# Optimization experiments

Hardware: AMD Instinct MI355X
Metric: run time of the kernel (lower is better)

Reference implementation:

```python
import jax, jax.numpy as jnp
from jax import lax
import numpy as np

D_MODEL = 1024
D_STATE = 64
D_CONV = 4
EXPAND = 2
HEADDIM = 64
D_INNER = EXPAND * D_MODEL          # 2048
NHEADS = D_INNER // HEADDIM         # 32
CHUNK = 64
CONV_DIM = D_INNER + 2 * D_STATE    # 2176
D_IN_PROJ = 2 * D_INNER + 2 * D_STATE + NHEADS  # 4256
B_SZ = 4
SEQLEN = 2048
EPS = 1e-5


def _silu(x):
    return x * jax.nn.sigmoid(x)


def _segsum(x):
    # x: [..., T]; returns [..., T, T] with [i,j] = sum_{j<k<=i} x[k], -inf above diag
    T = x.shape[-1]
    xe = jnp.broadcast_to(x[..., None], x.shape + (T,))
    strict_lower = jnp.tril(jnp.ones((T, T), bool), -1)
    xe = jnp.where(strict_lower, xe, 0.0)
    s = jnp.cumsum(xe, axis=-2)
    lower = jnp.tril(jnp.ones((T, T), bool), 0)
    return jnp.where(lower, s, -jnp.inf)


def setup_inputs() -> dict:
    key = jax.random.key(0)
    ks = jax.random.split(key, 5)
    u = jax.random.normal(ks[0], (B_SZ, SEQLEN, D_MODEL), jnp.float32)
    W_in = jax.random.normal(ks[1], (D_IN_PROJ, D_MODEL), jnp.float32) * 0.02
    conv_w = jax.random.normal(ks[2], (CONV_DIM, 1, D_CONV), jnp.float32) * 0.2  # depthwise kernel
    conv_b = jnp.zeros((CONV_DIM,), jnp.float32)
    dt_bias = jax.random.uniform(ks[3], (NHEADS,), jnp.float32, -1.0, 1.0)
    A_log = jnp.log(jnp.linspace(1.0, float(NHEADS), NHEADS)).astype(jnp.float32)
    D = jnp.ones((NHEADS,), jnp.float32)
    norm_w = jnp.ones((D_INNER,), jnp.float32)
    W_out = jax.random.normal(ks[4], (D_MODEL, D_INNER), jnp.float32) * 0.02
    return dict(u=u, W_in=W_in, conv_w=conv_w, conv_b=conv_b, dt_bias=dt_bias,
                A_log=A_log, D=D, norm_w=norm_w, W_out=W_out)


def reference(u, W_in, conv_w, conv_b, dt_bias, A_log, D, norm_w, W_out):
    b, s, _ = u.shape
    A = -jnp.exp(A_log)                                   # [H]
    zxbcdt = u @ W_in.T                                   # [b,s,D_IN_PROJ]
    z = zxbcdt[..., :D_INNER]
    xBC = zxbcdt[..., D_INNER:D_INNER + CONV_DIM]
    dt = jax.nn.softplus(zxbcdt[..., D_INNER + CONV_DIM:] + dt_bias)  # [b,s,H]

    # causal depthwise conv1d (left pad d_conv-1 == torch pad-both + slice[:s])
    xc = lax.conv_general_dilated(
        xBC.transpose(0, 2, 1), conv_w, window_strides=(1,),
        padding=[(D_CONV - 1, 0)], feature_group_count=CONV_DIM,
        dimension_numbers=('NCH', 'OIH', 'NCH'))
    xBC = _silu(xc.transpose(0, 2, 1) + conv_b)           # [b,s,CONV_DIM]

    x = xBC[..., :D_INNER].reshape(b, s, NHEADS, HEADDIM)
    Bm = xBC[..., D_INNER:D_INNER + D_STATE]              # [b,s,N]
    Cm = xBC[..., D_INNER + D_STATE:]                     # [b,s,N]

    # SSD chunked scan
    nch = s // CHUNK
    xs = (x * dt[..., None]).reshape(b, nch, CHUNK, NHEADS, HEADDIM)
    Ad = (A * dt).reshape(b, nch, CHUNK, NHEADS)
    Br = Bm.reshape(b, nch, CHUNK, D_STATE)
    Cr = Cm.reshape(b, nch, CHUNK, D_STATE)
    A_ch = Ad.transpose(0, 1, 3, 2)                       # [b,c,h,l]
    A_cum = jnp.cumsum(A_ch, axis=-1)
    L = jnp.exp(_segsum(A_ch))                            # [b,c,h,l,l]
    Y_diag = jnp.einsum('bcln,bcsn,bchls,bcshp->bclhp', Cr, Br, L, xs)
    decay_states = jnp.exp(A_cum[..., -1:] - A_cum)       # [b,c,h,l]
    states = jnp.einsum('bchl,bcln,bclhp->bchpn', decay_states, Br, xs)
    init = jnp.zeros((b, 1, NHEADS, HEADDIM, D_STATE), xs.dtype)
    states = jnp.concatenate([init, states], axis=1)      # [b,c+1,h,p,n]
    total_decay = jnp.pad(A_cum[..., -1].transpose(0, 2, 1), ((0, 0), (0, 0), (1, 0)))
    decay_chunk = jnp.exp(_segsum(total_decay))           # [b,h,c+1,c+1]
    new_states = jnp.einsum('bhzc,bchpn->bzhpn', decay_chunk, states)
    states = new_states[:, :-1]                           # [b,c,h,p,n]
    state_decay_out = jnp.exp(A_cum)
    Y_off = jnp.einsum('bcln,bchpn,bchl->bclhp', Cr, states, state_decay_out)
    y = (Y_diag + Y_off).reshape(b, s, NHEADS, HEADDIM)

    y = y + x * D[:, None]
    y = y.reshape(b, s, D_INNER)
    # gated RMSNorm
    y = y * _silu(z)
    y = y * lax.rsqrt(jnp.mean(y * y, axis=-1, keepdims=True) + EPS) * norm_w
    return y @ W_out.T
```

## Files before the change

### kernel.cpp

```cpp
#include <hip/hip_runtime.h>
#include <hip/hip_bf16.h>

#define BSZ 4
#define SEQ 2048
#define DMODEL 1024
#define DINNER 2048
#define DSTATE 64
#define NH 32
#define HD 64
#define CKL 64
#define NCH 32
#define CONVD 2176
#define DPROJ 4256
#define N1 4224
#define MTOT 8192
#define YSTR 72
#define YSTR2 120
#define CVTB 6272

typedef __hip_bfloat16 bf16;
typedef __attribute__((ext_vector_type(8))) short short8;
typedef __attribute__((ext_vector_type(4))) short short4_;
typedef __attribute__((ext_vector_type(4))) float f32x4;

__device__ __forceinline__ float sigmoidf_(float x) { return 1.0f / (1.0f + __expf(-x)); }
__device__ __forceinline__ float bits2f(short s) { return __uint_as_float(((unsigned)(unsigned short)s) << 16); }
__device__ __forceinline__ short f2bits(float f) {
    bf16 h = __float2bfloat16(f);
    return *reinterpret_cast<short*>(&h);
}

__device__ __forceinline__ void gl_lds16(const bf16* g, bf16* l) {
    __builtin_amdgcn_global_load_lds((const __attribute__((address_space(1))) void*)g,
                                     (__attribute__((address_space(3))) void*)l, 16, 0, 0);
}

__device__ __forceinline__ f32x4 MF(short8 a, short8 b, f32x4 c) {
    return __builtin_amdgcn_mfma_f32_16x16x32_bf16(a, b, c, 0, 0, 0);
}

template<int N> __device__ __forceinline__ void vmw() {
    if constexpr (N == 0)      asm volatile("s_waitcnt vmcnt(0)" ::: "memory");
    else if constexpr (N == 3) asm volatile("s_waitcnt vmcnt(3)" ::: "memory");
    else if constexpr (N == 6) asm volatile("s_waitcnt vmcnt(6)" ::: "memory");
    else                       asm volatile("s_waitcnt vmcnt(15)" ::: "memory");
}

__device__ __forceinline__ void swzx(int& bx, int& by) {
    int nx = gridDim.x;
    int nwg = nx * gridDim.y;
    int Lr = blockIdx.y * nx + blockIdx.x;
    int L = (Lr & 7) * (nwg >> 3) + (Lr >> 3);
    int GSZ = nx * 8;
    int g = L / GSZ, r = L - g * GSZ;
    bx = r % nx;
    by = g * 8 + r / nx;
}

__global__ __launch_bounds__(256) void k_pre2(const float* __restrict__ u, const float* __restrict__ W_in,
                                              const float* __restrict__ dt_bias,
                                              const float* __restrict__ W_out, const float* __restrict__ nw,
                                              bf16* __restrict__ u_b, float* __restrict__ dtt,
                                              bf16* __restrict__ win_b, bf16* __restrict__ wout_b) {
    __shared__ __align__(16) float us[8 * DMODEL];
    const int tid = threadIdx.x;
    if (blockIdx.x < CVTB) {
        int g = (blockIdx.x * 256 + tid) * 4;
        if (g < N1 * DMODEL) {
            f32x4 f = *(const f32x4*)&W_in[g];
            short4_ o;
#pragma unroll
            for (int j = 0; j < 4; j++) o[j] = f2bits(f[j]);
            *(short4_*)&win_b[g] = o;
        } else if (g < N1 * DMODEL + DMODEL * DINNER) {
            int g2 = g - N1 * DMODEL;
            f32x4 f = *(const f32x4*)&W_out[g2];
            f32x4 w = *(const f32x4*)&nw[g2 & (DINNER - 1)];
            short4_ o;
#pragma unroll
            for (int j = 0; j < 4; j++) o[j] = f2bits(f[j] * w[j]);
            *(short4_*)&wout_b[g2] = o;
        }
        return;
    }
    const int t0 = (blockIdx.x - CVTB) * 8;
    const float* ur = u + (size_t)t0 * DMODEL;
    bf16* ub = u_b + (size_t)t0 * DMODEL;
#pragma unroll
    for (int i = 0; i < 8; i++) {
        int idx = (i * 256 + tid) * 4;
        f32x4 v = *(const f32x4*)&ur[idx];
        *(f32x4*)&us[idx] = v;
        short4_ o;
#pragma unroll
        for (int j = 0; j < 4; j++) o[j] = f2bits(v[j]);
        *(short4_*)&ub[idx] = o;
    }
    __syncthreads();
    const int h = tid >> 3, sub = tid & 7;
    const float* wr = W_in + (size_t)(DPROJ - NH + h) * DMODEL;
    float s[8] = {};
    for (int k = sub * 4; k < DMODEL; k += 32) {
        f32x4 w4 = *(const f32x4*)&wr[k];
#pragma unroll
        for (int rr = 0; rr < 8; rr++) {
            f32x4 u4 = *(const f32x4*)&us[rr * DMODEL + k];
            s[rr] += u4[0] * w4[0] + u4[1] * w4[1] + u4[2] * w4[2] + u4[3] * w4[3];
        }
    }
#pragma unroll
    for (int rr = 0; rr < 8; rr++) {
        s[rr] += __shfl_down(s[rr], 4, 8);
        s[rr] += __shfl_down(s[rr], 2, 8);
        s[rr] += __shfl_down(s[rr], 1, 8);
    }
    if (sub == 0) {
        float bh = dt_bias[h];
#pragma unroll
        for (int rr = 0; rr < 8; rr++) {
            float x = s[rr] + bh;
            dtt[(size_t)h * MTOT + t0 + rr] = (x > 20.f) ? x : log1pf(__expf(x));
        }
    }
}

__global__ __launch_bounds__(256) void k_dts(const float* __restrict__ dtt, const float* __restrict__ A_log,
                                             float* __restrict__ sAc, float* __restrict__ sfv,
                                             float* __restrict__ etot) {
    const int h = blockIdx.x, b = blockIdx.y;
    const int tid = threadIdx.x, w = tid >> 6, lane = tid & 63;
    const float Ah = -__expf(A_log[h]);
#pragma unroll
    for (int g = 0; g < 8; g++) {
        int c = g * 4 + w;
        int t0 = b * SEQ + c * CKL;
        float dv = dtt[(size_t)h * MTOT + t0 + lane];
        float v = Ah * dv;
#pragma unroll
        for (int d = 1; d < 64; d <<= 1) { float o = __shfl_up(v, d); if (lane >= d) v += o; }
        float tot = __shfl(v, 63);
        sAc[(size_t)h * MTOT + t0 + lane] = v;
        sfv[(size_t)h * MTOT + t0 + lane] = __expf(tot - v) * dv;
        if (lane == 63) etot[(h * BSZ + b) * NCH + c] = __expf(tot);
    }
}

#define BARWAIT()                                           \
    __builtin_amdgcn_s_barrier();                           \
    asm volatile("s_waitcnt lgkmcnt(0)" ::: "memory");      \
    __builtin_amdgcn_sched_barrier(0);                      \
    __builtin_amdgcn_s_setprio(1)
#define ENDPH()                                             \
    __builtin_amdgcn_s_setprio(0);                          \
    __builtin_amdgcn_s_barrier()

__global__ __launch_bounds__(512, 2) void k_g1(const bf16* __restrict__ Ap,
                                               const bf16* __restrict__ Wp,
                                               bf16* __restrict__ Cp) {
    __shared__ __align__(16) short sA[2][16384];
    __shared__ __align__(16) short sB[2][12288];
    const int tid = threadIdx.x;
    const int lane = tid & 63, w = tid >> 6;
    const int wm = w >> 2, wn = w & 3;
    const int lr = lane & 15, lk = lane >> 4;
    int bx, by; swzx(bx, by);
    const int m0 = by * 256, n0 = bx * 192;
    const int ld = DMODEL;

    const int r8 = tid >> 3;
    const int c8 = ((tid & 7) ^ (r8 & 7)) * 8;
    const bf16* pA = Ap + (size_t)(m0 + r8) * ld + c8;
    const bf16* pB = Wp + (size_t)(n0 + r8) * ld + c8;

    auto stA = [&](int d, int t) {
#pragma unroll
        for (int h = 0; h < 2; h++)
#pragma unroll
            for (int q = 0; q < 2; q++)
                gl_lds16(pA + (size_t)(h * 128 + q * 64) * ld + t * 64,
                         (bf16*)&sA[d][h * 8192 + q * 4096 + tid * 8]);
    };
    auto stB = [&](int d, int u, int t) {
        gl_lds16(pB + (size_t)(u * 64) * ld + t * 64,
                 (bf16*)&sB[d][u * 4096 + tid * 8]);
    };

    const int c0 = (lk ^ (lr & 7)) * 8;
    const int c1 = ((lk + 4) ^ (lr & 7)) * 8;
    const int aR = (wm * 128 + lr) * 64;
    const int bR = (wn * 48 + lr) * 64;

    f32x4 acc[8][3];
#pragma unroll
    for (int i = 0; i < 8; i++)
#pragma unroll
        for (int j = 0; j < 3; j++) acc[i][j] = (f32x4){0.f, 0.f, 0.f, 0.f};
    short8 bfr[3][2], af[2][2];

#define RDA1(D, I)                                                   \
    af[0][0] = *(const short8*)&sA[D][aR + (I) * 1024 + c0];         \
    af[0][1] = *(const short8*)&sA[D][aR + (I) * 1024 + c1];         \
    af[1][0] = *(const short8*)&sA[D][aR + (I + 1) * 1024 + c0];     \
    af[1][1] = *(const short8*)&sA[D][aR + (I + 1) * 1024 + c1]
#define RDB1(D)                                                      \
    _Pragma("unroll")                                                \
    for (int jn = 0; jn < 3; ++jn) {                                 \
        bfr[jn][0] = *(const short8*)&sB[D][bR + jn * 1024 + c0];    \
        bfr[jn][1] = *(const short8*)&sB[D][bR + jn * 1024 + c1];    \
    }
#define MM1(I)                                                       \
    _Pragma("unroll")                                                \
    for (int hh = 0; hh < 2; ++hh) {                                 \
        _Pragma("unroll")                                            \
        for (int jn = 0; jn < 3; ++jn) {                             \
            acc[I][jn]     = MF(af[0][hh], bfr[jn][hh], acc[I][jn]); \
            acc[I + 1][jn] = MF(af[1][hh], bfr[jn][hh], acc[I + 1][jn]); \
        }                                                            \
    }

    stB(0, 0, 0); stB(0, 1, 0); stB(0, 2, 0); stA(0, 0);
    stB(1, 0, 1); stB(1, 1, 1); stB(1, 2, 1);
    vmw<3>();
    __builtin_amdgcn_s_barrier();

    for (int t0 = 0; t0 < 16; t0 += 2) {
        const int t1 = t0 + 1, t2 = t0 + 2, t3 = t0 + 3;
        const bool more = (t2 < 16);
        RDB1(0); RDA1(0, 0);
        stA(1, t1);
        BARWAIT(); MM1(0); ENDPH();
        RDA1(0, 2); if (more) stB(0, 0, t2);
        BARWAIT(); MM1(2); ENDPH();
        RDA1(0, 4); if (more) stB(0, 1, t2);
        BARWAIT(); MM1(4); ENDPH();
        RDA1(0, 6); if (more) stB(0, 2, t2);
        BARWAIT(); MM1(6);
        __builtin_amdgcn_s_setprio(0);
        if (more) vmw<3>(); else vmw<0>();
        __builtin_amdgcn_s_barrier();
        RDB1(1); RDA1(1, 0);
        if (more) stA(0, t2);
        BARWAIT(); MM1(0); ENDPH();
        RDA1(1, 2); if (more) stB(1, 0, t3);
        BARWAIT(); MM1(2); ENDPH();
        RDA1(1, 4); if (more) stB(1, 1, t3);
        BARWAIT(); MM1(4); ENDPH();
        RDA1(1, 6); if (more) stB(1, 2, t3);
        BARWAIT(); MM1(6);
        __builtin_amdgcn_s_setprio(0);
        if (more) vmw<3>();
        __builtin_amdgcn_s_barrier();
    }
#undef RDA1
#undef RDB1
#undef MM1

#pragma unroll
    for (int im = 0; im < 8; im++) {
        int row = m0 + wm * 128 + im * 16 + lk * 4;
#pragma unroll
        for (int jn = 0; jn < 3; jn++) {
            int col = n0 + wn * 48 + jn * 16 + lr;
            bf16* cp = Cp + (size_t)row * N1 + col;
#pragma unroll
            for (int rr = 0; rr < 4; rr++) cp[(size_t)rr * N1] = __float2bfloat16(acc[im][jn][rr]);
        }
    }
}

__global__ __launch_bounds__(512, 2) void k_g2(const bf16* __restrict__ Ap,
                                               const bf16* __restrict__ Wp,
                                               float* __restrict__ Cp) {
    __shared__ __align__(16) short sA[3][16384];
    __shared__ __align__(16) short sB[3][8192];
    __shared__ float rsrow[256];
    const int tid = threadIdx.x;
    const int lane = tid & 63, w = tid >> 6;
    const int wm = w >> 1, wn = w & 1;
    const int lr = lane & 15, lk = lane >> 4;
    int bx, by; swzx(bx, by);
    const int m0 = by * 256, n0 = bx * 128;
    const int lda = N1, ldb = DINNER;

    const int r8 = tid >> 3;
    const int c8 = ((tid & 7) ^ (r8 & 7)) * 8;
    const bf16* pA = Ap + (size_t)(m0 + r8) * lda + c8;
    const bf16* pB = Wp + (size_t)(n0 + r8) * ldb + c8;

    auto stA = [&](int d, int t) {
#pragma unroll
        for (int h = 0; h < 2; h++)
#pragma unroll
            for (int q = 0; q < 2; q++)
                gl_lds16(pA + (size_t)(h * 128 + q * 64) * lda + t * 64,
                         (bf16*)&sA[d][h * 8192 + q * 4096 + tid * 8]);
    };
    auto stB = [&](int d, int t) {
#pragma unroll
        for (int q = 0; q < 2; q++)
            gl_lds16(pB + (size_t)(q * 64) * ldb + t * 64,
                     (bf16*)&sB[d][q * 4096 + tid * 8]);
    };

    const int c0 = (lk ^ (lr & 7)) * 8;
    const int c1 = ((lk + 4) ^ (lr & 7)) * 8;
    const int aR = (wm * 64 + lr) * 64;
    const int bR = (wn * 64 + lr) * 64;

    f32x4 acc[4][4];
#pragma unroll
    for (int i = 0; i < 4; i++)
#pragma unroll
        for (int j = 0; j < 4; j++) acc[i][j] = (f32x4){0.f, 0.f, 0.f, 0.f};
    float ssq[4] = {0.f, 0.f, 0.f, 0.f};
    short8 bfr[4][2], af[2][2];

#define RDA2(D, I)                                                   \
    af[0][0] = *(const short8*)&sA[D][aR + (I) * 1024 + c0];         \
    af[0][1] = *(const short8*)&sA[D][aR + (I) * 1024 + c1];         \
    af[1][0] = *(const short8*)&sA[D][aR + (I + 1) * 1024 + c0];     \
    af[1][1] = *(const short8*)&sA[D][aR + (I + 1) * 1024 + c1]
#define RDB2(D)                                                      \
    _Pragma("unroll")                                                \
    for (int jn = 0; jn < 4; ++jn) {                                 \
        bfr[jn][0] = *(const short8*)&sB[D][bR + jn * 1024 + c0];    \
        bfr[jn][1] = *(const short8*)&sB[D][bR + jn * 1024 + c1];    \
    }
#define MM2(I)                                                       \
    _Pragma("unroll")                                                \
    for (int hh = 0; hh < 2; ++hh) {                                 \
        _Pragma("unroll")                                            \
        for (int jn = 0; jn < 4; ++jn) {                             \
            acc[I][jn]     = MF(af[0][hh], bfr[jn][hh], acc[I][jn]); \
            acc[I + 1][jn] = MF(af[1][hh], bfr[jn][hh], acc[I + 1][jn]); \
        }                                                            \
    }
#define SSQ2(I)                                                      \
    _Pragma("unroll")                                                \
    for (int hh = 0; hh < 2; ++hh)                                   \
        _Pragma("unroll")                                            \
        for (int e = 0; e < 8; ++e) {                                \
            float v0 = bits2f(af[0][hh][e]), v1 = bits2f(af[1][hh][e]); \
            ssq[I] += v0 * v0; ssq[I + 1] += v1 * v1;                \
        }

    stB(0, 0); stA(0, 0);
    stB(1, 1); stA(1, 1);
    vmw<6>();
    __builtin_amdgcn_s_barrier();

    int rb = 0, sb = 2;
    for (int t = 0; t < 32; ++t) {
        const bool more = (t + 2 < 32);
        RDB2(rb); RDA2(rb, 0);
        if (more) stB(sb, t + 2);
        BARWAIT(); MM2(0); SSQ2(0); ENDPH();
        RDA2(rb, 2);
        if (more) stA(sb, t + 2);
        BARWAIT(); MM2(2); SSQ2(2);
        __builtin_amdgcn_s_setprio(0);
        if (more) vmw<6>(); else if (t + 1 < 32) vmw<0>();
        __builtin_amdgcn_s_barrier();
        rb = (rb == 2) ? 0 : rb + 1;
        sb = (sb == 2) ? 0 : sb + 1;
    }
#undef RDA2
#undef RDB2
#undef MM2
#undef SSQ2

#pragma unroll
    for (int im = 0; im < 4; im++) {
        float s = ssq[im];
        s += __shfl_down(s, 32);
        s += __shfl_down(s, 16);
        if (lane < 16) rsrow[wm * 64 + im * 16 + lane] = rsqrtf(s * (1.0f / DINNER) + 1e-5f);
    }
    __syncthreads();
#pragma unroll
    for (int im = 0; im < 4; im++) {
        int rl = wm * 64 + im * 16 + lk * 4;
        int row = m0 + rl;
#pragma unroll
        for (int rr = 0; rr < 4; rr++) {
            float s = rsrow[rl + rr];
#pragma unroll
            for (int jn = 0; jn < 4; jn++) {
                int col = n0 + wn * 64 + jn * 16 + lr;
                Cp[(size_t)(row + rr) * DMODEL + col] = acc[im][jn][rr] * s;
            }
        }
    }
}

__global__ __launch_bounds__(256) void k_conv(const bf16* __restrict__ zx, const float* __restrict__ cw,
                                              const float* __restrict__ cb, bf16* __restrict__ xbc) {
    const int g = blockIdx.x * 256 + threadIdx.x;
    const int c0 = (g % 544) * 4;
    const int t0 = (g / 544) * 4;
    const int s0 = t0 & (SEQ - 1);
    const short* base = (const short*)(zx + (size_t)t0 * N1 + DINNER + c0);
    f32x4 w0 = *(const f32x4*)&cw[(c0 + 0) * 4];
    f32x4 w1 = *(const f32x4*)&cw[(c0 + 1) * 4];
    f32x4 w2 = *(const f32x4*)&cw[(c0 + 2) * 4];
    f32x4 w3 = *(const f32x4*)&cw[(c0 + 3) * 4];
    f32x4 bias = *(const f32x4*)&cb[c0];
    short4_ v[7];
#pragma unroll
    for (int o = 0; o < 7; o++) {
        if (s0 + o - 3 >= 0) v[o] = *(const short4_*)(base + (long)(o - 3) * N1);
        else v[o] = (short4_){0, 0, 0, 0};
    }
#pragma unroll
    for (int j = 0; j < 4; j++) {
        f32x4 a = bias;
#pragma unroll
        for (int k = 0; k < 4; k++) {
            short4_ x = v[j + k];
            a[0] += bits2f(x[0]) * w0[k];
            a[1] += bits2f(x[1]) * w1[k];
            a[2] += bits2f(x[2]) * w2[k];
            a[3] += bits2f(x[3]) * w3[k];
        }
        short4_ o_;
#pragma unroll
        for (int jj = 0; jj < 4; jj++) o_[jj] = f2bits(a[jj] * sigmoidf_(a[jj]));
        *(short4_*)((short*)xbc + (size_t)(t0 + j) * CONVD + c0) = o_;
    }
}

__global__ __launch_bounds__(256) void k_ssd(const bf16* __restrict__ xbc, const float* __restrict__ dtt,
                                             const float* __restrict__ sAc, const float* __restrict__ sfv,
                                             const float* __restrict__ etg, const float* __restrict__ Dp,
                                             bf16* __restrict__ zx) {
    __shared__ __align__(16) short Ct[2][64 * YSTR];
    __shared__ __align__(16) short Bt[2][64 * YSTR];
    __shared__ __align__(16) short Bn[2][64 * YSTR2];
    __shared__ __align__(16) short Xt[2][32 * YSTR2];
    __shared__ __align__(16) short Sb[2][32 * YSTR];
    __shared__ __align__(16) short Gs[4 * 16 * YSTR];
    __shared__ __align__(16) float Sf[32 * 68];
    __shared__ __align__(16) float sdt2[2][64], sAc2[2][64];
    __shared__ float etl[NCH];

    const int ph = blockIdx.x, h = blockIdx.y, b = blockIdx.z;
    const int tid = threadIdx.x;
    const int lane = tid & 63, w = tid >> 6;
    const int lr = lane & 15, lk = lane >> 4;
    const float Dh = Dp[h];
    const int xcol = h * HD + ph * 32;

    const int lrow = tid >> 2, c0 = (tid & 3) * 16, px = (tid & 3) * 8;
    const int zl = 16 * w + (lane >> 2), zp = (lane & 3) * 8;

    short8 rC0, rC1, rB0, rB1, rX, rZ;
    float rdt, rsa, rsf;
    auto load_chunk = [&](int cc) {
        int rows0 = b * SEQ + cc * CKL;
        const short* rp = (const short*)(xbc + (size_t)(rows0 + lrow) * CONVD);
        rC0 = *(const short8*)&rp[DINNER + DSTATE + c0];
        rC1 = *(const short8*)&rp[DINNER + DSTATE + c0 + 8];
        rB0 = *(const short8*)&rp[DINNER + c0];
        rB1 = *(const short8*)&rp[DINNER + c0 + 8];
        rX  = *(const short8*)&rp[xcol + px];
        rZ  = *(const short8*)((const short*)zx + (size_t)(rows0 + zl) * N1 + xcol + zp);
        rdt = dtt[(size_t)h * MTOT + rows0 + lane];
        rsa = sAc[(size_t)h * MTOT + rows0 + lane];
        rsf = sfv[(size_t)h * MTOT + rows0 + lrow];
    };
    auto scatter = [&](int buf) {
        *(short8*)&Ct[buf][lrow * YSTR + c0] = rC0;
        *(short8*)&Ct[buf][lrow * YSTR + c0 + 8] = rC1;
        *(short8*)&Bt[buf][lrow * YSTR + c0] = rB0;
        *(short8*)&Bt[buf][lrow * YSTR + c0 + 8] = rB1;
#pragma unroll
        for (int j = 0; j < 8; j++) {
            int n0_ = c0 + j, n1_ = c0 + 8 + j, p_ = px + j;
            Bn[buf][n0_ * YSTR2 + lrow + (n0_ >> 3) * 8] = f2bits(bits2f(rB0[j]) * rsf);
            Bn[buf][n1_ * YSTR2 + lrow + (n1_ >> 3) * 8] = f2bits(bits2f(rB1[j]) * rsf);
            Xt[buf][p_ * YSTR2 + lrow + (p_ >> 3) * 8] = rX[j];
        }
        if (tid < 64) { sdt2[buf][tid] = rdt; sAc2[buf][tid] = rsa; }
    };

    for (int i = tid; i < 32 * 68; i += 256) Sf[i] = 0.f;
    for (int i = tid; i < 32 * YSTR; i += 256) Sb[0][i] = 0;
    if (tid < NCH) etl[tid] = etg[(h * BSZ + b) * NCH + tid];
    load_chunk(0);
    scatter(0);
    __syncthreads();

    for (int c = 0; c < NCH; c++) {
        const int par = c & 1, nb = par ^ 1;
        const int rows0 = b * SEQ + c * CKL;
        float etot = etl[c];
        short8 zcur = rZ;
        if (c + 1 < NCH) load_chunk(c + 1);

        short8 cf0 = *(const short8*)&Ct[par][(16 * w + lr) * YSTR + lk * 8];
        short8 cf1 = *(const short8*)&Ct[par][(16 * w + lr) * YSTR + 32 + lk * 8];
        f32x4 acc[2];
#pragma unroll
        for (int t = 0; t < 2; t++) {
            short8 s0 = *(const short8*)&Sb[par][(16 * t + lr) * YSTR + lk * 8];
            short8 s1 = *(const short8*)&Sb[par][(16 * t + lr) * YSTR + 32 + lk * 8];
            acc[t] = MF(cf0, s0, (f32x4){0.f, 0.f, 0.f, 0.f});
            acc[t] = MF(cf1, s1, acc[t]);
        }
        float sAcl[4], el[4];
#pragma unroll
        for (int rr = 0; rr < 4; rr++) { sAcl[rr] = sAc2[par][16 * w + lk * 4 + rr]; el[rr] = __expf(sAcl[rr]); }
#pragma unroll
        for (int t = 0; t < 2; t++)
#pragma unroll
            for (int rr = 0; rr < 4; rr++) acc[t][rr] *= el[rr];
        short* gw = Gs + w * 16 * YSTR;
#pragma unroll
        for (int t = 0; t < 4; t++) {
            short8 b0 = *(const short8*)&Bt[par][(16 * t + lr) * YSTR + lk * 8];
            short8 b1 = *(const short8*)&Bt[par][(16 * t + lr) * YSTR + 32 + lk * 8];
            f32x4 g = MF(cf0, b0, (f32x4){0.f, 0.f, 0.f, 0.f});
            g = MF(cf1, b1, g);
            int s = 16 * t + lr;
            float sAcs = sAc2[par][s], dts = sdt2[par][s];
#pragma unroll
            for (int rr = 0; rr < 4; rr++) {
                int l = 16 * w + lk * 4 + rr;
                float v = (s <= l) ? g[rr] * __expf(sAcl[rr] - sAcs) * dts : 0.f;
                gw[(lk * 4 + rr) * YSTR + s] = f2bits(v);
            }
        }
        short8 gf0 = *(const short8*)&gw[lr * YSTR + lk * 8];
        short8 gf1 = *(const short8*)&gw[lr * YSTR + 32 + lk * 8];
#pragma unroll
        for (int t = 0; t < 2; t++) {
            int xr = 16 * t + lr;
            short8 x0 = *(const short8*)&Xt[par][xr * YSTR2 + ((xr >> 3) + lk) * 8];
            short8 x1 = *(const short8*)&Xt[par][xr * YSTR2 + 32 + ((xr >> 3) + lk) * 8];
            acc[t] = MF(gf0, x0, acc[t]);
            acc[t] = MF(gf1, x1, acc[t]);
        }
        {
            int pw = w & 1, nh2 = w >> 1;
            const int xp = 16 * pw + lr;
            short8 xt0 = *(const short8*)&Xt[par][xp * YSTR2 + ((xp >> 3) + lk) * 8];
            short8 xt1 = *(const short8*)&Xt[par][xp * YSTR2 + 32 + ((xp >> 3) + lk) * 8];
#pragma unroll
            for (int j = 0; j < 2; j++) {
                int nt = 2 * nh2 + j;
                int nr = 16 * nt + lr;
                short8 b0 = *(const short8*)&Bn[par][nr * YSTR2 + ((nr >> 3) + lk) * 8];
                short8 b1 = *(const short8*)&Bn[par][nr * YSTR2 + 32 + ((nr >> 3) + lk) * 8];
                f32x4 sacc = MF(xt0, b0, (f32x4){0.f, 0.f, 0.f, 0.f});
                sacc = MF(xt1, b1, sacc);
#pragma unroll
                for (int rr = 0; rr < 4; rr++) {
                    int n = 16 * nt + lr;
                    int p = 16 * pw + lk * 4 + rr;
                    float nv = Sf[p * 68 + n] * etot + sacc[rr];
                    Sf[p * 68 + n] = nv;
                    Sb[nb][p * YSTR + n] = f2bits(nv);
                }
            }
        }
#pragma unroll
        for (int t = 0; t < 2; t++) {
#pragma unroll
            for (int rr = 0; rr < 4; rr++) {
                int p = 16 * t + lr;
                int l = 16 * w + lk * 4 + rr;
                float y = acc[t][rr] + Dh * bits2f(Xt[par][p * YSTR2 + l + (p >> 3) * 8]);
                Ct[par][l * YSTR + p] = f2bits(y);
            }
        }
        {
            short8 y8 = *(const short8*)&Ct[par][zl * YSTR + zp];
            short* zpp = (short*)zx + (size_t)(rows0 + zl) * N1 + xcol + zp;
            short8 o;
#pragma unroll
            for (int j = 0; j < 8; j++) {
                float z = bits2f(zcur[j]);
                o[j] = f2bits(bits2f(y8[j]) * (z * sigmoidf_(z)));
            }
            *(short8*)zpp = o;
        }
        if (c + 1 < NCH) {
            scatter(nb);
        }
        __syncthreads();
    }
}

extern "C" void kernel_launch(void* const* d_in, const int* in_sizes, int n_in,
                              void* d_out, int out_size, void* d_ws, size_t ws_size,
                              hipStream_t stream) {
    const float* u       = (const float*)d_in[0];
    const float* W_in    = (const float*)d_in[1];
    const float* conv_w  = (const float*)d_in[2];
    const float* conv_b  = (const float*)d_in[3];
    const float* dt_bias = (const float*)d_in[4];
    const float* A_log   = (const float*)d_in[5];
    const float* Dp      = (const float*)d_in[6];
    const float* norm_w  = (const float*)d_in[7];
    const float* W_out   = (const float*)d_in[8];
    float* out = (float*)d_out;

    char* ws = (char*)d_ws;
    bf16* zx     = (bf16*)ws;  ws += (size_t)MTOT * N1 * 2;
    bf16* xbc    = (bf16*)ws;  ws += (size_t)MTOT * CONVD * 2;
    bf16* wout_b = (bf16*)ws;  ws += (size_t)DMODEL * DINNER * 2;
    float* dtt   = (float*)ws; ws += (size_t)NH * MTOT * 4;
    float* sAcw  = (float*)ws; ws += (size_t)NH * MTOT * 4;
    float* sfvw  = (float*)ws; ws += (size_t)NH * MTOT * 4;
    float* etotw = (float*)ws; ws += 64 * 1024;

    bf16* u_b   = (bf16*)d_out;
    bf16* win_b = (bf16*)((char*)d_out + (size_t)MTOT * DMODEL * 2);

    k_pre2<<<CVTB + MTOT / 8, 256, 0, stream>>>(u, W_in, dt_bias, W_out, norm_w,
                                                u_b, dtt, win_b, wout_b);
    k_dts<<<dim3(NH, BSZ), 256, 0, stream>>>(dtt, A_log, sAcw, sfvw, etotw);

    k_g1<<<dim3(N1 / 192, MTOT / 256), 512, 0, stream>>>(u_b, win_b, zx);

    k_conv<<<(MTOT / 4) * (CONVD / 4) / 256, 256, 0, stream>>>(zx, conv_w, conv_b, xbc);

    k_ssd<<<dim3(2, NH, BSZ), 256, 0, stream>>>(xbc, dtt, sAcw, sfvw, etotw, Dp, zx);

    k_g2<<<dim3(DMODEL / 128, MTOT / 256), 512, 0, stream>>>(zx, wout_b, out);
}
```

Before: 376.7 us.

## Fuse x-channel depthwise conv into SSD kernel, keep separate conv only for B/C

The depthwise conv+SiLU for the x channels now runs inside the SSD kernel's chunk loader, reading four shifted rows of the projection output directly. The standalone conv kernel only processes the 128 B/C channels into a compact buffer. This removes writing and re-reading a large intermediate xBC tensor. In exchange, the SSD kernel does extra loads and arithmetic per chunk, which may lengthen its critical path given its small grid.

```diff
diff --git a/kernel.cpp b/kernel.cpp
--- a/kernel.cpp
+++ b/kernel.cpp
@@ -393,18 +393,18 @@
     }
 }
 
-__global__ __launch_bounds__(256) void k_conv(const bf16* __restrict__ zx, const float* __restrict__ cw,
-                                              const float* __restrict__ cb, bf16* __restrict__ xbc) {
+__global__ __launch_bounds__(256) void k_convbc(const bf16* __restrict__ zx, const float* __restrict__ cw,
+                                                const float* __restrict__ cb, bf16* __restrict__ xbc_bc) {
     const int g = blockIdx.x * 256 + threadIdx.x;
-    const int c0 = (g % 544) * 4;
-    const int t0 = (g / 544) * 4;
+    const int c0 = (g & 31) * 4;
+    const int t0 = (g >> 5) * 4;
     const int s0 = t0 & (SEQ - 1);
-    const short* base = (const short*)(zx + (size_t)t0 * N1 + DINNER + c0);
-    f32x4 w0 = *(const f32x4*)&cw[(c0 + 0) * 4];
-    f32x4 w1 = *(const f32x4*)&cw[(c0 + 1) * 4];
-    f32x4 w2 = *(const f32x4*)&cw[(c0 + 2) * 4];
-    f32x4 w3 = *(const f32x4*)&cw[(c0 + 3) * 4];
-    f32x4 bias = *(const f32x4*)&cb[c0];
+    const short* base = (const short*)(zx + (size_t)t0 * N1 + DINNER + 2048 + c0);
+    f32x4 w0 = *(const f32x4*)&cw[(2048 + c0 + 0) * 4];
+    f32x4 w1 = *(const f32x4*)&cw[(2048 + c0 + 1) * 4];
+    f32x4 w2 = *(const f32x4*)&cw[(2048 + c0 + 2) * 4];
+    f32x4 w3 = *(const f32x4*)&cw[(2048 + c0 + 3) * 4];
+    f32x4 bias = *(const f32x4*)&cb[2048 + c0];
     short4_ v[7];
 #pragma unroll
     for (int o = 0; o < 7; o++) {
@@ -425,13 +425,15 @@
         short4_ o_;
 #pragma unroll
         for (int jj = 0; jj < 4; jj++) o_[jj] = f2bits(a[jj] * sigmoidf_(a[jj]));
-        *(short4_*)((short*)xbc + (size_t)(t0 + j) * CONVD + c0) = o_;
-    }
-}
-
-__global__ __launch_bounds__(256) void k_ssd(const bf16* __restrict__ xbc, const float* __restrict__ dtt,
+        *(short4_*)((short*)xbc_bc + (size_t)(t0 + j) * 128 + c0) = o_;
+    }
+}
+
+__global__ __launch_bounds__(256) void k_ssd(const bf16* __restrict__ zx_in, const bf16* __restrict__ xbc_bc,
+                                             const float* __restrict__ dtt,
                                              const float* __restrict__ sAc, const float* __restrict__ sfv,
                                              const float* __restrict__ etg, const float* __restrict__ Dp,
+                                             const float* __restrict__ cw, const float* __restrict__ cb,
                                              bf16* __restrict__ zx) {
     __shared__ __align__(16) short Ct[2][64 * YSTR];
     __shared__ __align__(16) short Bt[2][64 * YSTR];
@@ -453,16 +455,39 @@
     const int lrow = tid >> 2, c0 = (tid & 3) * 16, px = (tid & 3) * 8;
     const int zl = 16 * w + (lane >> 2), zp = (lane & 3) * 8;
 
+    f32x4 xw[8]; f32x4 xb0, xb1;
+#pragma unroll
+    for (int j = 0; j < 8; j++) xw[j] = *(const f32x4*)&cw[(xcol + px + j) * 4];
+    xb0 = *(const f32x4*)&cb[xcol + px];
+    xb1 = *(const f32x4*)&cb[xcol + px + 4];
+
     short8 rC0, rC1, rB0, rB1, rX, rZ;
     float rdt, rsa, rsf;
     auto load_chunk = [&](int cc) {
         int rows0 = b * SEQ + cc * CKL;
-        const short* rp = (const short*)(xbc + (size_t)(rows0 + lrow) * CONVD);
-        rC0 = *(const short8*)&rp[DINNER + DSTATE + c0];
-        rC1 = *(const short8*)&rp[DINNER + DSTATE + c0 + 8];
-        rB0 = *(const short8*)&rp[DINNER + c0];
-        rB1 = *(const short8*)&rp[DINNER + c0 + 8];
-        rX  = *(const short8*)&rp[xcol + px];
+        const short* rp = (const short*)(xbc_bc + (size_t)(rows0 + lrow) * 128);
+        rB0 = *(const short8*)&rp[c0];
+        rB1 = *(const short8*)&rp[c0 + 8];
+        rC0 = *(const short8*)&rp[64 + c0];
+        rC1 = *(const short8*)&rp[64 + c0 + 8];
+        {
+            int rt = rows0 + lrow;
+            int s = rt & (SEQ - 1);
+            const short* xg = (const short*)zx_in + (size_t)rt * N1 + DINNER + xcol + px;
+            short8 tp[4];
+#pragma unroll
+            for (int k = 0; k < 4; k++) {
+                tp[k] = (s + k - 3 >= 0) ? *(const short8*)(xg + (long)(k - 3) * N1)
+                                         : (short8){0, 0, 0, 0, 0, 0, 0, 0};
+            }
+#pragma unroll
+            for (int j = 0; j < 8; j++) {
+                float a = (j < 4) ? xb0[j] : xb1[j - 4];
+#pragma unroll
+                for (int k = 0; k < 4; k++) a += bits2f(tp[k][j]) * xw[j][k];
+                rX[j] = f2bits(a * sigmoidf_(a));
+            }
+        }
         rZ  = *(const short8*)((const short*)zx + (size_t)(rows0 + zl) * N1 + xcol + zp);
         rdt = dtt[(size_t)h * MTOT + rows0 + lane];
         rsa = sAc[(size_t)h * MTOT + rows0 + lane];
@@ -607,7 +632,7 @@
 
     char* ws = (char*)d_ws;
     bf16* zx     = (bf16*)ws;  ws += (size_t)MTOT * N1 * 2;
-    bf16* xbc    = (bf16*)ws;  ws += (size_t)MTOT * CONVD * 2;
+    bf16* xbc_bc = (bf16*)ws;  ws += (size_t)MTOT * 128 * 2;
     bf16* wout_b = (bf16*)ws;  ws += (size_t)DMODEL * DINNER * 2;
     float* dtt   = (float*)ws; ws += (size_t)NH * MTOT * 4;
     float* sAcw  = (float*)ws; ws += (size_t)NH * MTOT * 4;
@@ -623,9 +648,10 @@
 
     k_g1<<<dim3(N1 / 192, MTOT / 256), 512, 0, stream>>>(u_b, win_b, zx);
 
-    k_conv<<<(MTOT / 4) * (CONVD / 4) / 256, 256, 0, stream>>>(zx, conv_w, conv_b, xbc);
-
-    k_ssd<<<dim3(2, NH, BSZ), 256, 0, stream>>>(xbc, dtt, sAcw, sfvw, etotw, Dp, zx);
+    k_convbc<<<(MTOT / 4) * (128 / 4) / 256, 256, 0, stream>>>(zx, conv_w, conv_b, xbc_bc);
+
+    k_ssd<<<dim3(2, NH, BSZ), 256, 0, stream>>>(zx, xbc_bc, dtt, sAcw, sfvw, etotw, Dp,
+                                                conv_w, conv_b, zx);
 
     k_g2<<<dim3(DMODEL / 128, MTOT / 256), 512, 0, stream>>>(zx, wout_b, out);
 }
```

Measured after the change: 385.7 us. +2.4%, slower.
